# Optimization experiments

Hardware: AMD Instinct MI355X
Metric: run time of the kernel (lower is better)

Reference implementation:

```python
import jax, jax.numpy as jnp
import numpy as np

B, S, D, H = 2, 2048, 2048, 16
HD = D // H  # head dim = 128


def setup_inputs() -> dict:
    key = jax.random.key(0)
    ks = jax.random.split(key, 9)
    sc = 1.0 / np.sqrt(D)
    return {
        "hidden_states": jax.random.normal(ks[0], (B, S, D), jnp.float32),
        "Wq": jax.random.normal(ks[1], (D, D), jnp.float32) * sc,
        "bq": jax.random.normal(ks[2], (D,), jnp.float32) * 0.02,
        "Wk": jax.random.normal(ks[3], (D, D), jnp.float32) * sc,
        "bk": jax.random.normal(ks[4], (D,), jnp.float32) * 0.02,
        "Wv": jax.random.normal(ks[5], (D, D), jnp.float32) * sc,
        "bv": jax.random.normal(ks[6], (D,), jnp.float32) * 0.02,
        "Wo": jax.random.normal(ks[7], (D, D), jnp.float32) * sc,
        "bo": jax.random.normal(ks[8], (D,), jnp.float32) * 0.02,
    }


def _rotate_half(x):
    x1, x2 = jnp.split(x, 2, axis=-1)
    return jnp.concatenate((-x2, x1), axis=-1)


def reference(hidden_states, Wq, bq, Wk, bk, Wv, bv, Wo, bo):
    b, s, d = hidden_states.shape
    # QKV projections (torch Linear: x @ W.T + b)
    def proj(W, bias):
        y = jnp.einsum('bsd,ed->bse', hidden_states, W) + bias
        return y.reshape(b, s, H, HD).transpose(0, 2, 1, 3)  # [B,H,S,HD]
    q, k, v = proj(Wq, bq), proj(Wk, bk), proj(Wv, bv)

    # Rotary embedding tables
    inv_freq = 1.0 / (10000.0 ** (jnp.arange(0, HD, 2, dtype=jnp.float32) / HD))
    t = jnp.arange(s, dtype=jnp.float32)
    freqs = jnp.einsum('i,j->ij', t, inv_freq)          # [S, HD/2]
    emb = jnp.concatenate((freqs, freqs), axis=-1)       # [S, HD]
    cos_cached, sin_cached = jnp.cos(emb), jnp.sin(emb)
    # NOTE: source unpacks `sin, cos = rotary_emb(...)` while forward returns
    # (cos, sin) -> swap is intentional to match original math.
    sin_t, cos_t = cos_cached, sin_cached
    q = q * cos_t + _rotate_half(q) * sin_t
    k = k * cos_t + _rotate_half(k) * sin_t

    scores = jnp.einsum('bhsd,bhtd->bhst', q, k) / jnp.sqrt(jnp.float32(HD))
    probs = jax.nn.softmax(scores, axis=-1)
    ctx = jnp.einsum('bhst,bhtd->bhsd', probs, v)
    ctx = ctx.transpose(0, 2, 1, 3).reshape(b, s, d)
    return jnp.einsum('bsd,ed->bse', ctx, Wo) + bo
```

## Files before the change

kernel.cpp:

```cpp
#include <hip/hip_runtime.h>

constexpr int NH = 16;
constexpr int SEQ = 2048;
constexpr int DMODEL = 2048;
constexpr int HDIM = 128;
constexpr int NB = 2;
constexpr int MTOT = NB * SEQ;
constexpr long NEL = (long)NB * SEQ * DMODEL;
constexpr long WEL = (long)DMODEL * DMODEL;
constexpr size_t FUSED_WS = 2ul * (4 * NEL + 3 * WEL + 12288);

typedef __attribute__((ext_vector_type(8))) __bf16 bf16x8;
typedef __attribute__((ext_vector_type(4))) float f32x4;

__device__ __forceinline__ float bf2f(ushort u) {
  union { uint i; float f; } v; v.i = ((uint)u) << 16; return v.f;
}
__device__ __forceinline__ ushort f2bf(float f) {
  union { float f; uint i; } v; v.f = f;
  uint r = (v.i + 0x7FFFu + ((v.i >> 16) & 1u)) >> 16;
  return (ushort)r;
}
__device__ __forceinline__ ushort f2bf_rhu(float f) {
  union { float f; uint i; } v; v.f = f;
  return (ushort)((v.i + 0x8000u) >> 16);
}

__global__ __launch_bounds__(256) void conv_f32_bf16(
    const float* __restrict__ s, ushort* __restrict__ d, int n4) {
  const int i = blockIdx.x * 256 + threadIdx.x;
  if (i < n4) {
    const float4 v = ((const float4*)s)[i];
    ushort4 o;
    o.x = f2bf(v.x); o.y = f2bf(v.y); o.z = f2bf(v.z); o.w = f2bf(v.w);
    ((ushort4*)d)[i] = o;
  }
}

__global__ __launch_bounds__(256) void bias_cat(
    const float* __restrict__ a, const float* __restrict__ b,
    const float* __restrict__ c, float* __restrict__ o) {
  const int i = blockIdx.x * 256 + threadIdx.x;
  o[i] = (i < 2048) ? a[i] : (i < 4096) ? b[i - 2048] : c[i - 4096];
}

template <int MODE>
__global__ __launch_bounds__(256) void gemm_bt(
    const ushort* __restrict__ A, const ushort* __restrict__ Bw,
    const float* __restrict__ bias, void* __restrict__ Cv,
    int M, int N, int K) {
  __shared__ __align__(16) ushort lA[128 * 32];
  __shared__ __align__(16) ushort lB[128 * 32];
  const int tid = threadIdx.x;
  const int wave = tid >> 6, lane = tid & 63;
  const int quad = lane >> 4, l16 = lane & 15;
  const int nb = N >> 7;
  const int bm = blockIdx.x / nb, bn = blockIdx.x % nb;
  const int m0 = bm << 7, n0 = bn << 7;
  const int wm = (wave >> 1) << 6, wn = (wave & 1) << 6;

  f32x4 acc[4][4] = {};

  const int srow = lane >> 2;
  const int schk = (lane & 3) << 3;
  const ushort* gA = A + (long)(m0 + wave * 32 + srow) * K + schk;
  const ushort* gB = Bw + (long)(n0 + wave * 32 + srow) * K + schk;
  ushort* sA = lA + (wave * 32) * 32;
  ushort* sB = lB + (wave * 32) * 32;

  for (int k0 = 0; k0 < K; k0 += 32) {
    __syncthreads();
    __builtin_amdgcn_global_load_lds(
        (const __attribute__((address_space(1))) void*)(gA + k0),
        (__attribute__((address_space(3))) void*)sA, 16, 0, 0);
    __builtin_amdgcn_global_load_lds(
        (const __attribute__((address_space(1))) void*)(gA + k0 + 16L * K),
        (__attribute__((address_space(3))) void*)(sA + 16 * 32), 16, 0, 0);
    __builtin_amdgcn_global_load_lds(
        (const __attribute__((address_space(1))) void*)(gB + k0),
        (__attribute__((address_space(3))) void*)sB, 16, 0, 0);
    __builtin_amdgcn_global_load_lds(
        (const __attribute__((address_space(1))) void*)(gB + k0 + 16L * K),
        (__attribute__((address_space(3))) void*)(sB + 16 * 32), 16, 0, 0);
    __syncthreads();

    bf16x8 af[4], bfr[4];
#pragma unroll
    for (int i = 0; i < 4; i++) {
      af[i]  = *(const bf16x8*)(lA + (wm + i * 16 + l16) * 32 + (quad << 3));
      bfr[i] = *(const bf16x8*)(lB + (wn + i * 16 + l16) * 32 + (quad << 3));
    }
#pragma unroll
    for (int mi = 0; mi < 4; mi++)
#pragma unroll
      for (int ni = 0; ni < 4; ni++)
        acc[mi][ni] = __builtin_amdgcn_mfma_f32_16x16x32_bf16(
            af[mi], bfr[ni], acc[mi][ni], 0, 0, 0);
  }

#pragma unroll
  for (int ni = 0; ni < 4; ni++) {
    const int col = n0 + wn + ni * 16 + l16;
    const float bv = bias[col];
#pragma unroll
    for (int mi = 0; mi < 4; mi++) {
#pragma unroll
      for (int r = 0; r < 4; r++) {
        const int row = m0 + wm + mi * 16 + quad * 4 + r;
        const float v = acc[mi][ni][r] + bv;
        if (MODE == 0) {
          ((float*)Cv)[(long)row * N + col] = v;
        } else {
          const int b = row >> 11, s = row & (SEQ - 1);
          const int h = (col >> 7) & 15, hd = col & (HDIM - 1);
          const long off = (long)(col >> 11) * NEL +
              ((long)(b * NH + h) * SEQ + s) * HDIM + hd;
          ((ushort*)Cv)[off] = f2bf(v);
        }
      }
    }
  }
}

__global__ __launch_bounds__(256) void rope_qk(ushort* Q, ushort* Kt) {
  const int gid = blockIdx.x * 256 + threadIdx.x;
  const int n = gid & 4194303;
  const bool isK = (gid >= 4194304);
  ushort* ptr = isK ? Kt : Q;
  const float qs = isK ? 1.0f : 0.08838834764831845f;
  const int p = n & 63;
  const int s = (n >> 6) & (SEQ - 1);
  const int bh = n >> 17;
  const long idx = (long)bh * (SEQ * HDIM) + (long)s * HDIM + p;
  const float invf = exp2f(-(float)p * 0.2076205059304601f);
  const float f = (float)s * invf;
  float sn, cs;
  sincosf(f, &sn, &cs);
  const float x1 = bf2f(ptr[idx]);
  const float x2 = bf2f(ptr[idx + 64]);
  ptr[idx]      = f2bf((x1 * sn - x2 * cs) * qs);
  ptr[idx + 64] = f2bf((x2 * sn + x1 * cs) * qs);
}

__global__ __launch_bounds__(256) void transpose_v(const ushort* __restrict__ V,
                                                   ushort* __restrict__ VT) {
  __shared__ ushort lT[64 * 65];
  const int bh = blockIdx.x >> 6;
  const int rem = blockIdx.x & 63;
  const int t0 = (rem >> 1) << 6, d0 = (rem & 1) << 6;
  const ushort* vb = V + (long)bh * (SEQ * HDIM);
  ushort* ob = VT + (long)bh * (SEQ * HDIM);
  const int tid = threadIdx.x;
#pragma unroll
  for (int it = 0; it < 16; it++) {
    const int idx = it * 256 + tid;
    const int r = idx >> 6, c = idx & 63;
    lT[c * 65 + r] = vb[(long)(t0 + r) * HDIM + d0 + c];
  }
  __syncthreads();
#pragma unroll
  for (int it = 0; it < 16; it++) {
    const int idx = it * 256 + tid;
    const int r = idx >> 6, c = idx & 63;
    ob[(long)(d0 + r) * SEQ + t0 + c] = lT[r * 65 + c];
  }
}

__global__ __launch_bounds__(256) void attn(const ushort* __restrict__ Q,
                                            const ushort* __restrict__ Kp,
                                            const ushort* __restrict__ VT,
                                            ushort* __restrict__ ctx) {
  __shared__ __align__(16) ushort smem[23040];
  ushort* lK = smem;
  ushort* lV = smem + 64 * 136;
  ushort* lP = smem + 64 * 136 + 128 * 72;
  const int tid = threadIdx.x;
  const int wave = tid >> 6, lane = tid & 63;
  const int quad = lane >> 4, l16 = lane & 15;
  const int xcd = blockIdx.x & 7, loc = blockIdx.x >> 3;
  const int bh = xcd * 4 + (loc >> 5), qt = loc & 31;
  const long hb = (long)bh * (SEQ * HDIM);
  const int b = bh >> 4, h = bh & 15;
  const int qh = wave & 1, th = wave >> 1;
  ushort* myP = lP + wave * (32 * 40);

  bf16x8 qa[2][4];
#pragma unroll
  for (int qq = 0; qq < 2; qq++)
#pragma unroll
    for (int c = 0; c < 4; c++)
      qa[qq][c] = *(const bf16x8*)(
          Q + hb + (long)(qt * 64 + qh * 32 + qq * 16 + l16) * HDIM +
          c * 32 + (quad << 3));

  f32x4 o[2][8] = {};
  f32x4 lacc[2] = {};
  bf16x8 ones;
#pragma unroll
  for (int i = 0; i < 8; i++) ones[i] = (__bf16)1.0f;

  const ushort* kSrc = Kp + hb + (long)(tid >> 4) * HDIM + (tid & 15) * 8;
  const ushort* vSrc = VT + hb + (long)(tid >> 3) * SEQ + (tid & 7) * 8;
  ushort* kDst = lK + (tid >> 4) * 136 + (tid & 15) * 8;
  ushort* vDst = lV + (tid >> 3) * 72 + (tid & 7) * 8;
  const ushort* kRow = lK + (th * 32 + l16) * 136 + (quad << 3);
  const ushort* vRow = lV + l16 * 72 + th * 32 + (quad << 3);
  const ushort* pRow = myP + l16 * 40 + (quad << 3);
  ushort* pWr = myP + l16 * 40 + (quad << 2);

  for (int t0 = 0; t0 < SEQ; t0 += 64) {
    __syncthreads();
#pragma unroll
    for (int it = 0; it < 4; it++) {
      *(bf16x8*)(kDst + it * (16 * 136)) =
          *(const bf16x8*)(kSrc + (long)it * (16 * HDIM));
      *(bf16x8*)(vDst + it * (32 * 72)) =
          *(const bf16x8*)(vSrc + (long)it * (32 * SEQ));
    }
    kSrc += 64 * HDIM;
    vSrc += 64;
    __syncthreads();

    f32x4 st[2][2] = {};
#pragma unroll
    for (int kc = 0; kc < 4; kc++)
#pragma unroll
      for (int tt = 0; tt < 2; tt++) {
        const bf16x8 ka = *(const bf16x8*)(kRow + tt * (16 * 136) + kc * 32);
#pragma unroll
        for (int qq = 0; qq < 2; qq++)
          st[tt][qq] = __builtin_amdgcn_mfma_f32_16x16x32_bf16(
              ka, qa[qq][kc], st[tt][qq], 0, 0, 0);
      }

#pragma unroll
    for (int qq = 0; qq < 2; qq++)
#pragma unroll
      for (int tt = 0; tt < 2; tt++)
#pragma unroll
        for (int r = 0; r < 4; r++)
          pWr[qq * (16 * 40) + tt * 16 + r] = f2bf_rhu(__expf(st[tt][qq][r]));

    __syncthreads();

    bf16x8 pa[2];
#pragma unroll
    for (int qq = 0; qq < 2; qq++) {
      pa[qq] = *(const bf16x8*)(pRow + qq * (16 * 40));
      lacc[qq] = __builtin_amdgcn_mfma_f32_16x16x32_bf16(
          pa[qq], ones, lacc[qq], 0, 0, 0);
    }
#pragma unroll
    for (int nt = 0; nt < 8; nt++) {
      const bf16x8 vb = *(const bf16x8*)(vRow + nt * (16 * 72));
#pragma unroll
      for (int qq = 0; qq < 2; qq++)
        o[qq][nt] = __builtin_amdgcn_mfma_f32_16x16x32_bf16(
            pa[qq], vb, o[qq][nt], 0, 0, 0);
    }
  }

  __syncthreads();
  float* mb = (float*)smem;
  if (wave >= 2) {
    float* p = mb + ((wave - 2) * 64 + lane) * 73;
#pragma unroll
    for (int qq = 0; qq < 2; qq++) {
#pragma unroll
      for (int nt = 0; nt < 8; nt++)
#pragma unroll
        for (int r = 0; r < 4; r++) p[qq * 32 + nt * 4 + r] = o[qq][nt][r];
#pragma unroll
      for (int r = 0; r < 4; r++) p[64 + qq * 4 + r] = lacc[qq][r];
    }
  }
  __syncthreads();
  if (wave < 2) {
    const float* p = mb + (wave * 64 + lane) * 73;
#pragma unroll
    for (int qq = 0; qq < 2; qq++) {
#pragma unroll
      for (int nt = 0; nt < 8; nt++)
#pragma unroll
        for (int r = 0; r < 4; r++) o[qq][nt][r] += p[qq * 32 + nt * 4 + r];
#pragma unroll
      for (int r = 0; r < 4; r++) lacc[qq][r] += p[64 + qq * 4 + r];
    }
#pragma unroll
    for (int qq = 0; qq < 2; qq++)
#pragma unroll
      for (int r = 0; r < 4; r++) {
        const float inv = 1.0f / lacc[qq][r];
        const int s = qt * 64 + qh * 32 + qq * 16 + quad * 4 + r;
        const long base = ((long)(b * SEQ + s)) * DMODEL + h * HDIM;
#pragma unroll
        for (int nt = 0; nt < 8; nt++)
          ctx[base + nt * 16 + l16] = f2bf(o[qq][nt][r] * inv);
      }
  }
}

extern "C" void kernel_launch(void* const* d_in, const int* in_sizes, int n_in,
                              void* d_out, int out_size, void* d_ws, size_t ws_size,
                              hipStream_t stream) {
  const float* hid = (const float*)d_in[0];
  const float* Wq = (const float*)d_in[1];
  const float* bq = (const float*)d_in[2];
  const float* Wk = (const float*)d_in[3];
  const float* bk = (const float*)d_in[4];
  const float* Wv = (const float*)d_in[5];
  const float* bv = (const float*)d_in[6];
  const float* Wo = (const float*)d_in[7];
  const float* bo = (const float*)d_in[8];
  float* out = (float*)d_out;
  ushort* ws = (ushort*)d_ws;

  ushort* qw   = ws;
  ushort* kw   = ws + NEL;
  ushort* vw   = ws + 2 * NEL;
  ushort* hidB = ws + 3 * NEL;
  ushort* wB   = ws + 4 * NEL;

  dim3 blk(256);
  conv_f32_bf16<<<(int)(NEL / 4 / 256), blk, 0, stream>>>(hid, hidB, NEL / 4);

  if (ws_size >= FUSED_WS) {
    conv_f32_bf16<<<(int)(WEL / 4 / 256), blk, 0, stream>>>(Wq, wB, WEL / 4);
    conv_f32_bf16<<<(int)(WEL / 4 / 256), blk, 0, stream>>>(Wk, wB + WEL, WEL / 4);
    conv_f32_bf16<<<(int)(WEL / 4 / 256), blk, 0, stream>>>(Wv, wB + 2 * WEL, WEL / 4);
    float* bc = (float*)(wB + 3 * WEL);
    bias_cat<<<24, blk, 0, stream>>>(bq, bk, bv, bc);
    gemm_bt<1><<<1536, blk, 0, stream>>>(hidB, wB, bc, qw, MTOT, 3 * DMODEL, DMODEL);
  } else {
    conv_f32_bf16<<<(int)(WEL / 4 / 256), blk, 0, stream>>>(Wq, wB, WEL / 4);
    gemm_bt<1><<<512, blk, 0, stream>>>(hidB, wB, bq, qw, MTOT, DMODEL, DMODEL);
    conv_f32_bf16<<<(int)(WEL / 4 / 256), blk, 0, stream>>>(Wk, wB, WEL / 4);
    gemm_bt<1><<<512, blk, 0, stream>>>(hidB, wB, bk, kw, MTOT, DMODEL, DMODEL);
    conv_f32_bf16<<<(int)(WEL / 4 / 256), blk, 0, stream>>>(Wv, wB, WEL / 4);
    gemm_bt<1><<<512, blk, 0, stream>>>(hidB, wB, bv, vw, MTOT, DMODEL, DMODEL);
  }

  rope_qk<<<32768, blk, 0, stream>>>(qw, kw);

  ushort* vtw = hidB;
  transpose_v<<<2048, blk, 0, stream>>>(vw, vtw);

  ushort* cw = vw;
  attn<<<1024, blk, 0, stream>>>(qw, kw, vtw, cw);

  conv_f32_bf16<<<(int)(WEL / 4 / 256), blk, 0, stream>>>(Wo, wB, WEL / 4);
  gemm_bt<0><<<512, blk, 0, stream>>>(cw, wB, bo, out, MTOT, DMODEL, DMODEL);
}
```

Baseline: 502.2 us.

## Replace GEMM with 256x256-tile double-buffered, swizzled-LDS, 8-wave pipelined kernel

Replaces the 128x128, single-buffered GEMM with a 256x256-tile kernel using 512 threads and 128KB of LDS. The K-loop is double-buffered with interleaved global-to-LDS staging and MFMA phases, controlled by explicit vmcnt waits, barriers and setprio. LDS uses XOR swizzling to avoid bank conflicts, and block indices are remapped across groups of 8. The aim is to hide memory latency and raise data reuse per tile for the QKV and output projections. In exchange, grids become small (128 or 384 blocks), so the 128-block launches may underfill the CUs, and the hand-ordered waits are fragile.

```diff
diff --git a/kernel.cpp b/kernel.cpp
--- a/kernel.cpp
+++ b/kernel.cpp
@@ -44,82 +44,146 @@
   o[i] = (i < 2048) ? a[i] : (i < 4096) ? b[i - 2048] : c[i - 4096];
 }
 
+#define GLDS(src, dst)                                              \
+  __builtin_amdgcn_global_load_lds(                                 \
+      (const __attribute__((address_space(1))) void*)(src),         \
+      (__attribute__((address_space(3))) void*)(dst), 16, 0, 0)
+
+#define STAGE_A(d, mh, kc) do {                                     \
+    const ushort* _s = gA + (long)((mh) * 128) * K + (kc) * 64;     \
+    ushort* _d = smem + (d) * 16384 + (mh) * 8192 + w * 1024;       \
+    GLDS(_s, _d);                                                   \
+    GLDS(_s + 8 * (long)K, _d + 512);                               \
+  } while (0)
+
+#define STAGE_B(d, nh, kc) do {                                     \
+    const ushort* _s = gB + (long)((nh) * 128) * K + (kc) * 64;     \
+    ushort* _d = smem + 32768 + (d) * 16384 + (nh) * 8192 + w * 1024; \
+    GLDS(_s, _d);                                                   \
+    GLDS(_s + 8 * (long)K, _d + 512);                               \
+  } while (0)
+
+#define LDA(d, mh) do {                                             \
+    const ushort* _p = smem + (d) * 16384 + (mh) * 8192 +           \
+                       (wm * 64 + l16) * 64;                        \
+    _Pragma("unroll")                                               \
+    for (int _i = 0; _i < 4; _i++) {                                \
+      afr[_i][0] = *(const bf16x8*)(_p + _i * 1024 + sw0);          \
+      afr[_i][1] = *(const bf16x8*)(_p + _i * 1024 + sw1);          \
+    }                                                               \
+  } while (0)
+
+#define LDB(d, nh) do {                                             \
+    const ushort* _p = smem + 32768 + (d) * 16384 + (nh) * 8192 +   \
+                       (wn * 32 + l16) * 64;                        \
+    _Pragma("unroll")                                               \
+    for (int _j = 0; _j < 2; _j++) {                                \
+      bfr[nh][_j][0] = *(const bf16x8*)(_p + _j * 1024 + sw0);      \
+      bfr[nh][_j][1] = *(const bf16x8*)(_p + _j * 1024 + sw1);      \
+    }                                                               \
+  } while (0)
+
+#define MMA(mh, nh) do {                                            \
+    __builtin_amdgcn_s_setprio(1);                                  \
+    _Pragma("unroll")                                               \
+    for (int _i = 0; _i < 4; _i++)                                  \
+      _Pragma("unroll")                                             \
+      for (int _j = 0; _j < 2; _j++) {                              \
+        acc[mh][_i][nh][_j] = __builtin_amdgcn_mfma_f32_16x16x32_bf16( \
+            afr[_i][0], bfr[nh][_j][0], acc[mh][_i][nh][_j], 0, 0, 0); \
+        acc[mh][_i][nh][_j] = __builtin_amdgcn_mfma_f32_16x16x32_bf16( \
+            afr[_i][1], bfr[nh][_j][1], acc[mh][_i][nh][_j], 0, 0, 0); \
+      }                                                             \
+    __builtin_amdgcn_s_setprio(0);                                  \
+  } while (0)
+
+#define BARX() __builtin_amdgcn_s_barrier()
+#define WAITV(n) asm volatile("s_waitcnt vmcnt(" #n ")" ::: "memory")
+#define WAITL() asm volatile("s_waitcnt lgkmcnt(0)" ::: "memory")
+
 template <int MODE>
-__global__ __launch_bounds__(256) void gemm_bt(
+__global__ __launch_bounds__(512, 2) void gemm256(
     const ushort* __restrict__ A, const ushort* __restrict__ Bw,
     const float* __restrict__ bias, void* __restrict__ Cv,
     int M, int N, int K) {
-  __shared__ __align__(16) ushort lA[128 * 32];
-  __shared__ __align__(16) ushort lB[128 * 32];
+  __shared__ __align__(16) ushort smem[65536];
   const int tid = threadIdx.x;
-  const int wave = tid >> 6, lane = tid & 63;
+  const int w = tid >> 6, lane = tid & 63;
   const int quad = lane >> 4, l16 = lane & 15;
-  const int nb = N >> 7;
-  const int bm = blockIdx.x / nb, bn = blockIdx.x % nb;
-  const int m0 = bm << 7, n0 = bn << 7;
-  const int wm = (wave >> 1) << 6, wn = (wave & 1) << 6;
-
-  f32x4 acc[4][4] = {};
-
-  const int srow = lane >> 2;
-  const int schk = (lane & 3) << 3;
-  const ushort* gA = A + (long)(m0 + wave * 32 + srow) * K + schk;
-  const ushort* gB = Bw + (long)(n0 + wave * 32 + srow) * K + schk;
-  ushort* sA = lA + (wave * 32) * 32;
-  ushort* sB = lB + (wave * 32) * 32;
-
-  for (int k0 = 0; k0 < K; k0 += 32) {
-    __syncthreads();
-    __builtin_amdgcn_global_load_lds(
-        (const __attribute__((address_space(1))) void*)(gA + k0),
-        (__attribute__((address_space(3))) void*)sA, 16, 0, 0);
-    __builtin_amdgcn_global_load_lds(
-        (const __attribute__((address_space(1))) void*)(gA + k0 + 16L * K),
-        (__attribute__((address_space(3))) void*)(sA + 16 * 32), 16, 0, 0);
-    __builtin_amdgcn_global_load_lds(
-        (const __attribute__((address_space(1))) void*)(gB + k0),
-        (__attribute__((address_space(3))) void*)sB, 16, 0, 0);
-    __builtin_amdgcn_global_load_lds(
-        (const __attribute__((address_space(1))) void*)(gB + k0 + 16L * K),
-        (__attribute__((address_space(3))) void*)(sB + 16 * 32), 16, 0, 0);
-    __syncthreads();
-
-    bf16x8 af[4], bfr[4];
+  const int wm = w >> 2, wn = w & 3;
+  const int nbn = N >> 8;
+  const int cpx = (int)gridDim.x >> 3;
+  const int swz = (blockIdx.x & 7) * cpx + (blockIdx.x >> 3);
+  const int bm = swz / nbn, bn = swz % nbn;
+  const int m0 = bm << 8, n0 = bn << 8;
+  const int KT = K >> 6;
+
+  const int srow = (w << 4) + (lane >> 3);
+  const int scol = ((lane & 7) ^ (lane >> 3)) << 3;
+  const ushort* gA = A + (long)(m0 + srow) * K + scol;
+  const ushort* gB = Bw + (long)(n0 + srow) * K + scol;
+  const int sw0 = ((quad ^ (lane & 7)) << 3);
+  const int sw1 = (((4 + quad) ^ (lane & 7)) << 3);
+
+  f32x4 acc[2][4][2][2] = {};
+  bf16x8 afr[4][2];
+  bf16x8 bfr[2][2][2];
+
+  STAGE_A(0, 0, 0); STAGE_B(0, 0, 0); STAGE_B(0, 1, 0); STAGE_A(0, 1, 0);
+  STAGE_A(1, 0, 1); STAGE_B(1, 0, 1);
+  WAITV(4);
+  BARX();
+
+  for (int t = 0; t < KT; t += 2) {
+    const int c2 = (t + 2 < KT) ? t + 2 : 0;
+    const int c3 = (t + 3 < KT) ? t + 3 : (t + 3 - KT);
+    STAGE_B(1, 1, t + 1); WAITV(6); BARX();
+    LDA(0, 0); LDB(0, 0); WAITL();
+    MMA(0, 0); BARX();
+    LDB(0, 1); STAGE_A(1, 1, t + 1); BARX(); WAITL();
+    MMA(0, 1); BARX();
+    LDA(0, 1); STAGE_A(0, 0, c2); BARX(); WAITL();
+    MMA(1, 0); BARX();
+    STAGE_B(0, 0, c2); BARX();
+    MMA(1, 1); BARX();
+    STAGE_B(0, 1, c2); WAITV(6); BARX();
+    LDA(1, 0); LDB(1, 0); WAITL();
+    MMA(0, 0); BARX();
+    LDB(1, 1); STAGE_A(0, 1, c2); BARX(); WAITL();
+    MMA(0, 1); BARX();
+    LDA(1, 1); STAGE_A(1, 0, c3); BARX(); WAITL();
+    MMA(1, 0); BARX();
+    STAGE_B(1, 0, c3); BARX();
+    MMA(1, 1); BARX();
+  }
+
+#pragma unroll
+  for (int mh = 0; mh < 2; mh++)
 #pragma unroll
     for (int i = 0; i < 4; i++) {
-      af[i]  = *(const bf16x8*)(lA + (wm + i * 16 + l16) * 32 + (quad << 3));
-      bfr[i] = *(const bf16x8*)(lB + (wn + i * 16 + l16) * 32 + (quad << 3));
-    }
-#pragma unroll
-    for (int mi = 0; mi < 4; mi++)
-#pragma unroll
-      for (int ni = 0; ni < 4; ni++)
-        acc[mi][ni] = __builtin_amdgcn_mfma_f32_16x16x32_bf16(
-            af[mi], bfr[ni], acc[mi][ni], 0, 0, 0);
-  }
-
-#pragma unroll
-  for (int ni = 0; ni < 4; ni++) {
-    const int col = n0 + wn + ni * 16 + l16;
-    const float bv = bias[col];
-#pragma unroll
-    for (int mi = 0; mi < 4; mi++) {
-#pragma unroll
-      for (int r = 0; r < 4; r++) {
-        const int row = m0 + wm + mi * 16 + quad * 4 + r;
-        const float v = acc[mi][ni][r] + bv;
-        if (MODE == 0) {
-          ((float*)Cv)[(long)row * N + col] = v;
-        } else {
-          const int b = row >> 11, s = row & (SEQ - 1);
-          const int h = (col >> 7) & 15, hd = col & (HDIM - 1);
-          const long off = (long)(col >> 11) * NEL +
-              ((long)(b * NH + h) * SEQ + s) * HDIM + hd;
-          ((ushort*)Cv)[off] = f2bf(v);
+      const int rbase = m0 + mh * 128 + wm * 64 + i * 16 + quad * 4;
+#pragma unroll
+      for (int nh = 0; nh < 2; nh++)
+#pragma unroll
+        for (int j = 0; j < 2; j++) {
+          const int col = n0 + nh * 128 + wn * 32 + j * 16 + l16;
+          const float bv = bias[col];
+#pragma unroll
+          for (int r = 0; r < 4; r++) {
+            const int row = rbase + r;
+            const float v = acc[mh][i][nh][j][r] + bv;
+            if (MODE == 0) {
+              ((float*)Cv)[(long)row * N + col] = v;
+            } else {
+              const int b = row >> 11, s = row & (SEQ - 1);
+              const int h = (col >> 7) & 15, hd = col & (HDIM - 1);
+              const long off = (long)(col >> 11) * NEL +
+                  ((long)(b * NH + h) * SEQ + s) * HDIM + hd;
+              ((ushort*)Cv)[off] = f2bf(v);
+            }
+          }
         }
-      }
-    }
-  }
+    }
 }
 
 __global__ __launch_bounds__(256) void rope_qk(ushort* Q, ushort* Kt) {
@@ -322,6 +386,7 @@
   ushort* wB   = ws + 4 * NEL;
 
   dim3 blk(256);
+  dim3 blkG(512);
   conv_f32_bf16<<<(int)(NEL / 4 / 256), blk, 0, stream>>>(hid, hidB, NEL / 4);
 
   if (ws_size >= FUSED_WS) {
@@ -330,14 +395,14 @@
     conv_f32_bf16<<<(int)(WEL / 4 / 256), blk, 0, stream>>>(Wv, wB + 2 * WEL, WEL / 4);
     float* bc = (float*)(wB + 3 * WEL);
     bias_cat<<<24, blk, 0, stream>>>(bq, bk, bv, bc);
-    gemm_bt<1><<<1536, blk, 0, stream>>>(hidB, wB, bc, qw, MTOT, 3 * DMODEL, DMODEL);
+    gemm256<1><<<384, blkG, 0, stream>>>(hidB, wB, bc, qw, MTOT, 3 * DMODEL, DMODEL);
   } else {
     conv_f32_bf16<<<(int)(WEL / 4 / 256), blk, 0, stream>>>(Wq, wB, WEL / 4);
-    gemm_bt<1><<<512, blk, 0, stream>>>(hidB, wB, bq, qw, MTOT, DMODEL, DMODEL);
+    gemm256<1><<<128, blkG, 0, stream>>>(hidB, wB, bq, qw, MTOT, DMODEL, DMODEL);
     conv_f32_bf16<<<(int)(WEL / 4 / 256), blk, 0, stream>>>(Wk, wB, WEL / 4);
-    gemm_bt<1><<<512, blk, 0, stream>>>(hidB, wB, bk, kw, MTOT, DMODEL, DMODEL);
+    gemm256<1><<<128, blkG, 0, stream>>>(hidB, wB, bk, kw, MTOT, DMODEL, DMODEL);
     conv_f32_bf16<<<(int)(WEL / 4 / 256), blk, 0, stream>>>(Wv, wB, WEL / 4);
-    gemm_bt<1><<<512, blk, 0, stream>>>(hidB, wB, bv, vw, MTOT, DMODEL, DMODEL);
+    gemm256<1><<<128, blkG, 0, stream>>>(hidB, wB, bv, vw, MTOT, DMODEL, DMODEL);
   }
 
   rope_qk<<<32768, blk, 0, stream>>>(qw, kw);
@@ -349,5 +414,5 @@
   attn<<<1024, blk, 0, stream>>>(qw, kw, vtw, cw);
 
   conv_f32_bf16<<<(int)(WEL / 4 / 256), blk, 0, stream>>>(Wo, wB, WEL / 4);
-  gemm_bt<0><<<512, blk, 0, stream>>>(cw, wB, bo, out, MTOT, DMODEL, DMODEL);
-}
+  gemm256<0><<<128, blkG, 0, stream>>>(cw, wB, bo, out, MTOT, DMODEL, DMODEL);
+}
```

New measurement: 453.9 us. -9.6%, faster.
